# Optimization experiments

Hardware: AMD Instinct MI355X
Metric: run time of the kernel (lower is better)

The kernel has to match this reference:

```python
import jax, jax.numpy as jnp
import numpy as np
import math

B, S, D, H = 2, 2048, 1024, 16
DH = D // H  # head_dim = 64
NEG = -10000.0


def setup_inputs() -> dict:
    key = jax.random.key(0)
    ks = jax.random.split(key, 6)
    scale = 1.0 / math.sqrt(D)
    inp = {
        "query": jax.random.normal(ks[0], (B, S, D), dtype=jnp.float32),
        "key": jax.random.normal(ks[1], (B, S, D), dtype=jnp.float32),
        "value": jax.random.normal(ks[2], (B, S, D), dtype=jnp.float32),
        "Wq": jax.random.normal(ks[3], (D, D), dtype=jnp.float32) * scale,
        "Wk": jax.random.normal(ks[4], (D, D), dtype=jnp.float32) * scale,
        "Wv": jax.random.normal(ks[5], (D, D), dtype=jnp.float32) * scale,
        "pad_mask": jnp.ones((B, 1, 1, S), dtype=jnp.int32),
        "attn_mask": jnp.tril(jnp.ones((S, S), dtype=jnp.int32))[None, None],  # causal [1,1,S,S]
    }
    return inp


def reference(query, key, value, Wq, Wk, Wv, pad_mask, attn_mask):
    b, s, d = query.shape
    # torch Linear(bias=False): y = x @ W.T ; then split into heads [B,H,S,DH]
    def proj(x, W):
        return (x @ W.T).reshape(b, -1, H, DH).transpose(0, 2, 1, 3)

    Q = proj(query, Wq)
    K = proj(key, Wk)
    V = proj(value, Wv)

    scores = jnp.einsum("bhqd,bhkd->bhqk", Q, K) / math.sqrt(DH)
    scores = jnp.where(attn_mask == 0, NEG, scores)
    scores = jnp.where(pad_mask == 0, NEG, scores)
    attn = jax.nn.softmax(scores, axis=-1)  # dropout p=0.0 -> identity
    ctx = jnp.einsum("bhqk,bhkd->bhqd", attn, V)
    return ctx.transpose(0, 2, 1, 3).reshape(b, -1, d)
```

## Files before the change

### kernel.cpp

```cpp
#include <hip/hip_runtime.h>


typedef unsigned short u16;
typedef unsigned int u32;
typedef u16 u16x4 __attribute__((ext_vector_type(4)));
typedef u16 u16x8 __attribute__((ext_vector_type(8)));
typedef u32 u32x2 __attribute__((ext_vector_type(2)));
typedef u32 u32x4 __attribute__((ext_vector_type(4)));
typedef __bf16 bf16x8 __attribute__((ext_vector_type(8)));
typedef float f32x4 __attribute__((ext_vector_type(4)));

static __device__ __forceinline__ u16 f2bf(float f) {
  unsigned u = __builtin_bit_cast(unsigned, f);
  return (u16)((u + 0x7FFFu + ((u >> 16) & 1u)) >> 16);
}

static __device__ __forceinline__ u32 cvt_pk_bf16(float lo, float hi) {
  u32 r;
  asm("v_cvt_pk_bf16_f32 %0, %1, %2" : "=v"(r) : "v"(lo), "v"(hi));
  return r;
}

static __device__ __forceinline__ u16x8 cvt8(float4 f0, float4 f1) {
  u32x4 v;
  v[0] = cvt_pk_bf16(f0.x, f0.y);
  v[1] = cvt_pk_bf16(f0.z, f0.w);
  v[2] = cvt_pk_bf16(f1.x, f1.y);
  v[3] = cvt_pk_bf16(f1.z, f1.w);
  return __builtin_bit_cast(u16x8, v);
}

static __device__ __forceinline__ f32x4 mfma16(u16x8 a, u16x8 b, f32x4 c) {
  return __builtin_amdgcn_mfma_f32_16x16x32_bf16(
      __builtin_bit_cast(bf16x8, a), __builtin_bit_cast(bf16x8, b), c, 0, 0, 0);
}

#define GLOAD16(GSRC, LDST)                                                  \
  __builtin_amdgcn_global_load_lds(                                         \
      (const __attribute__((address_space(1))) unsigned int*)(GSRC),        \
      (__attribute__((address_space(3))) unsigned int*)(LDST), 16, 0, 0)

#define FENCE() asm volatile("" ::: "memory")
#define BARX()                        \
  do {                                \
    __builtin_amdgcn_s_barrier();     \
    FENCE();                          \
  } while (0)

__global__ __launch_bounds__(256) void wconv_kernel(
    const float* __restrict__ Wq, const float* __restrict__ Wk,
    const float* __restrict__ Wv, u16* __restrict__ dst) {
  const float* src = (blockIdx.y == 0) ? Wq : (blockIdx.y == 1) ? Wk : Wv;
  u16* d = dst + (size_t)blockIdx.y * (1024 * 1024);
  const int i = (blockIdx.x * 256 + threadIdx.x) * 8;
  const float4 f0 = *(const float4*)(src + i);
  const float4 f1 = *(const float4*)(src + i + 4);
  *(u16x8*)(d + i) = cvt8(f0, f1);
}

__global__ __launch_bounds__(256) void proj_kernel(
    const float* __restrict__ Xq, const float* __restrict__ Xk, const float* __restrict__ Xv,
    const u16* __restrict__ Wbf,
    u16* __restrict__ Qb, u16* __restrict__ Kb, u16* __restrict__ Vt) {
  const int d0 = blockIdx.x;
  const int tid = (d0 & 7) * 96 + (d0 >> 3);
  const int nI = tid % 24, mI = tid / 24;
  const int mode = nI >> 3;
  const int m0 = mI * 128;
  const int n0 = (nI & 7) * 128;

  const float* __restrict__ X = (mode == 0) ? Xq : (mode == 1) ? Xk : Xv;
  const u16* __restrict__ W = Wbf + (size_t)mode * (1024 * 1024);

  __shared__ __align__(16) u16 As[3][128 * 32];
  __shared__ __align__(16) u16 Bs[3][128 * 32];

  const int t = threadIdx.x;
  const int lane = t & 63;
  const int w = t >> 6;
  const int wm = w >> 1, wn = w & 1;
  const int lr = lane & 15, lg = lane >> 4;

  const int srow0 = w * 32 + (lane >> 2);
  const int srow1 = srow0 + 16;
  const int skoff = ((lane & 3) ^ ((lane >> 3) & 3)) * 8;
  const int ldsb0 = w * 2048 + lane * 16;
  const int ldsb1 = ldsb0 + 1024;

  const float* Xr0 = X + (size_t)(m0 + srow0) * 1024 + skoff;
  const float* Xr1 = X + (size_t)(m0 + srow1) * 1024 + skoff;
  const u16* Wr0 = W + (size_t)(n0 + srow0) * 1024 + skoff;
  const u16* Wr1 = W + (size_t)(n0 + srow1) * 1024 + skoff;

  float4 a0_, a1_, a2_, a3_;

#define ISSUE_A(T)                                   \
  do {                                               \
    const float* _p0 = Xr0 + (T) * 32;               \
    const float* _p1 = Xr1 + (T) * 32;               \
    a0_ = ((const float4*)_p0)[0];                   \
    a1_ = ((const float4*)_p0)[1];                   \
    a2_ = ((const float4*)_p1)[0];                   \
    a3_ = ((const float4*)_p1)[1];                   \
  } while (0)
#define WRITE_A(BUF)                                                 \
  do {                                                               \
    *(u16x8*)((char*)As[BUF] + ldsb0) = cvt8(a0_, a1_);              \
    *(u16x8*)((char*)As[BUF] + ldsb1) = cvt8(a2_, a3_);              \
  } while (0)
#define ISSUE_B(T, BUF)                                              \
  do {                                                               \
    GLOAD16(Wr0 + (T) * 32, (char*)Bs[BUF] + w * 2048);              \
    GLOAD16(Wr1 + (T) * 32, (char*)Bs[BUF] + w * 2048 + 1024);       \
  } while (0)

  f32x4 acc[4][4] = {};
  const int rx = (lr >> 1) & 3;

#define CMP(BUF)                                                              \
  do {                                                                       \
    u16x8 af[4], bfr[4];                                                     \
    _Pragma("unroll") for (int mi = 0; mi < 4; ++mi) {                        \
      const int row = wm * 64 + mi * 16 + lr;                                \
      af[mi] = *(const u16x8*)((char*)As[BUF] + row * 64 + ((lg ^ rx) << 4)); \
    }                                                                         \
    _Pragma("unroll") for (int ni = 0; ni < 4; ++ni) {                        \
      const int row = wn * 64 + ni * 16 + lr;                                \
      bfr[ni] = *(const u16x8*)((char*)Bs[BUF] + row * 64 + ((lg ^ rx) << 4));\
    }                                                                         \
    _Pragma("unroll") for (int mi = 0; mi < 4; ++mi)                          \
        _Pragma("unroll") for (int ni = 0; ni < 4; ++ni)                      \
            acc[mi][ni] = mfma16(af[mi], bfr[ni], acc[mi][ni]);               \
  } while (0)

  ISSUE_A(0); WRITE_A(0);
  ISSUE_A(1); WRITE_A(1);
  ISSUE_A(2);
  ISSUE_B(0, 0);
  ISSUE_B(1, 1);
  asm volatile("s_waitcnt vmcnt(2) lgkmcnt(0)" ::: "memory");
  BARX();

  CMP(0);
  BARX();
  WRITE_A(2);
  ISSUE_A(3);
  ISSUE_B(2, 2);

  for (int tt = 1; tt <= 29; ++tt) {
    asm volatile("s_waitcnt vmcnt(6) lgkmcnt(0)" ::: "memory");
    BARX();
    CMP(tt % 3);
    BARX();
    WRITE_A((tt + 2) % 3);
    if (tt < 29) ISSUE_A(tt + 3);
    ISSUE_B(tt + 2, (tt + 2) % 3);
  }

  asm volatile("s_waitcnt vmcnt(2) lgkmcnt(0)" ::: "memory");
  BARX();
  CMP(30 % 3);
  asm volatile("s_waitcnt vmcnt(0) lgkmcnt(0)" ::: "memory");
  BARX();
  CMP(31 % 3);
#undef ISSUE_A
#undef WRITE_A
#undef ISSUE_B
#undef CMP

#pragma unroll
  for (int mi = 0; mi < 4; ++mi) {
    const int sbase = m0 + wm * 64 + mi * 16 + lg * 4;
    const int b_ = sbase >> 11;
    const int s_ = sbase & 2047;
#pragma unroll
    for (int ni = 0; ni < 4; ++ni) {
      const int n = n0 + wn * 64 + ni * 16 + lr;
      const int h_ = n >> 6, dh = n & 63;
      if (mode == 2) {
        u16x4 pk;
        pk[0] = f2bf(acc[mi][ni][0]);
        pk[1] = f2bf(acc[mi][ni][1]);
        pk[2] = f2bf(acc[mi][ni][2]);
        pk[3] = f2bf(acc[mi][ni][3]);
        *(u16x4*)(Vt + ((size_t)((b_ * 16 + h_) * 64 + dh)) * 2048 + s_) = pk;
      } else {
        const float sc = (mode == 0) ? 0.18033688f : 1.0f;
        u16* dst = (mode == 0 ? Qb : Kb) + (size_t)(b_ * 16 + h_) * (2048 * 64) + dh;
#pragma unroll
        for (int r = 0; r < 4; ++r)
          dst[(size_t)(s_ + r) * 64] = f2bf(acc[mi][ni][r] * sc);
      }
    }
  }
}

__global__ __launch_bounds__(256, 4) void attn_kernel(
    const u16* __restrict__ Qb, const u16* __restrict__ Kb, const u16* __restrict__ Vt,
    const int* __restrict__ pad, float* __restrict__ out) {
  const int bh = blockIdx.x;
  const int qb = blockIdx.y;
  const int b = bh >> 4, h = bh & 15;
  const int q0 = qb * 64;
  const u16* Qh = Qb + (size_t)bh * (2048 * 64);
  const u16* Kh = Kb + (size_t)bh * (2048 * 64);
  const u16* Vh = Vt + (size_t)bh * (64 * 2048);
  const int* padb = pad + b * 2048;

  __shared__ u16 Ks[2][64 * 64];
  __shared__ u16 Vs[2][64 * 64];
  __shared__ u16 Ps[4][16 * 64];

  const int t = threadIdx.x, lane = t & 63, w = t >> 6;
  const int lr = lane & 15, lg = lane >> 4;
  const int swz = (lr & 7) << 4;
  const int sr = t >> 3, scb = t & 7;
  const int qwave = q0 + w * 16;
  const int qlane = qwave + lr;
  const int nsteps = qb + 1;

  u16x8 qf[2];
#pragma unroll
  for (int kc = 0; kc < 2; ++kc)
    qf[kc] = *(const u16x8*)(Qh + (size_t)qlane * 64 + kc * 32 + lg * 8);

  f32x4 acc[4] = {};
  float mrow = -1e4f, lsum = 0.f;

  u16x8 kr0, kr1, vr0, vr1;
  const int sb0 = (sr * 128 + scb * 16) ^ ((sr & 7) << 4);
  const int sb1 = ((32 + sr) * 128 + scb * 16) ^ ((sr & 7) << 4);

  kr0 = *(const u16x8*)(Kh + (size_t)sr * 64 + scb * 8);
  kr1 = *(const u16x8*)(Kh + (size_t)(32 + sr) * 64 + scb * 8);
  vr0 = *(const u16x8*)(Vh + (size_t)sr * 2048 + scb * 8);
  vr1 = *(const u16x8*)(Vh + (size_t)(32 + sr) * 2048 + scb * 8);
  *(u16x8*)((char*)Ks[0] + sb0) = kr0;
  *(u16x8*)((char*)Ks[0] + sb1) = kr1;
  *(u16x8*)((char*)Vs[0] + sb0) = vr0;
  *(u16x8*)((char*)Vs[0] + sb1) = vr1;
  __syncthreads();

  int cur = 0;
  for (int st = 0; st < nsteps; ++st) {
    const int kv0 = st << 6;
    const bool more = st + 1 < nsteps;
    if (more) {
      const int nv0 = kv0 + 64;
      kr0 = *(const u16x8*)(Kh + (size_t)(nv0 + sr) * 64 + scb * 8);
      kr1 = *(const u16x8*)(Kh + (size_t)(nv0 + 32 + sr) * 64 + scb * 8);
      vr0 = *(const u16x8*)(Vh + (size_t)sr * 2048 + nv0 + scb * 8);
      vr1 = *(const u16x8*)(Vh + (size_t)(32 + sr) * 2048 + nv0 + scb * 8);
    }
    int4 pv4[4];
#pragma unroll
    for (int ct = 0; ct < 4; ++ct)
      pv4[ct] = *(const int4*)(padb + kv0 + ct * 16 + lg * 4);

    const u16* KsC = Ks[cur];
    const u16* VsC = Vs[cur];

    f32x4 s4[4] = {};
#pragma unroll
    for (int ct = 0; ct < 4; ++ct) {
      if (kv0 + ct * 16 <= qwave + 15) {
#pragma unroll
        for (int kc = 0; kc < 2; ++kc) {
          const int byt = ((ct * 16 + lr) * 128 + kc * 64 + lg * 16) ^ swz;
          const u16x8 kf = *(const u16x8*)((char*)KsC + byt);
          s4[ct] = mfma16(kf, qf[kc], s4[ct]);
        }
      }
    }

    float vv[4][4];
    const int pall = pv4[0].x & pv4[0].y & pv4[0].z & pv4[0].w &
                     pv4[1].x & pv4[1].y & pv4[1].z & pv4[1].w &
                     pv4[2].x & pv4[2].y & pv4[2].z & pv4[2].w &
                     pv4[3].x & pv4[3].y & pv4[3].z & pv4[3].w;
    if ((kv0 + 63 <= qwave) && __all(pall != 0)) {
#pragma unroll
      for (int ct = 0; ct < 4; ++ct)
#pragma unroll
        for (int r = 0; r < 4; ++r) vv[ct][r] = s4[ct][r];
    } else {
      const int lim = qlane - kv0 - lg * 4;
#pragma unroll
      for (int ct = 0; ct < 4; ++ct) {
        const int* pvp = (const int*)&pv4[ct];
#pragma unroll
        for (int r = 0; r < 4; ++r)
          vv[ct][r] = (pvp[r] && (ct * 16 + r) <= lim) ? s4[ct][r] : -1e4f;
      }
    }

    float m0 = fmaxf(fmaxf(fmaxf(vv[0][0], vv[0][1]), fmaxf(vv[0][2], vv[0][3])),
                     fmaxf(fmaxf(vv[1][0], vv[1][1]), fmaxf(vv[1][2], vv[1][3])));
    float m1 = fmaxf(fmaxf(fmaxf(vv[2][0], vv[2][1]), fmaxf(vv[2][2], vv[2][3])),
                     fmaxf(fmaxf(vv[3][0], vv[3][1]), fmaxf(vv[3][2], vv[3][3])));
    float mx = fmaxf(m0, m1);
    mx = fmaxf(mx, __shfl_xor(mx, 16));
    mx = fmaxf(mx, __shfl_xor(mx, 32));
    const float mn = fmaxf(mrow, mx);
    const float al = exp2f(mrow - mn);
    mrow = mn;

    float p[4][4];
#pragma unroll
    for (int ct = 0; ct < 4; ++ct)
#pragma unroll
      for (int r = 0; r < 4; ++r) p[ct][r] = exp2f(vv[ct][r] - mn);
    float ps = (((p[0][0] + p[0][1]) + (p[0][2] + p[0][3])) +
                ((p[1][0] + p[1][1]) + (p[1][2] + p[1][3]))) +
               (((p[2][0] + p[2][1]) + (p[2][2] + p[2][3])) +
                ((p[3][0] + p[3][1]) + (p[3][2] + p[3][3])));
    ps += __shfl_xor(ps, 16);
    ps += __shfl_xor(ps, 32);
    lsum = lsum * al + ps;

    u16* PsB = &Ps[w][0];
#pragma unroll
    for (int ct = 0; ct < 4; ++ct) {
      u32x2 pw;
      pw[0] = cvt_pk_bf16(p[ct][0], p[ct][1]);
      pw[1] = cvt_pk_bf16(p[ct][2], p[ct][3]);
      const int pb = (lr * 128 + ct * 32 + lg * 8) ^ swz;
      *(u32x2*)((char*)PsB + pb) = pw;
    }
    const u16x8 pa0 = *(const u16x8*)((char*)PsB + ((lr * 128 + lg * 16) ^ swz));
    const u16x8 pa1 = *(const u16x8*)((char*)PsB + ((lr * 128 + 64 + lg * 16) ^ swz));

    float alv[4];
#pragma unroll
    for (int r = 0; r < 4; ++r)
      alv[r] = __builtin_bit_cast(
          float, __builtin_amdgcn_ds_bpermute((lg * 4 + r) * 4, __builtin_bit_cast(int, al)));

#pragma unroll
    for (int dt = 0; dt < 4; ++dt) {
#pragma unroll
      for (int r = 0; r < 4; ++r) acc[dt][r] *= alv[r];
      const int r0 = (dt * 16 + lr) * 128;
      acc[dt] = mfma16(pa0, *(const u16x8*)((char*)VsC + ((r0 + lg * 16) ^ swz)), acc[dt]);
      acc[dt] = mfma16(pa1, *(const u16x8*)((char*)VsC + ((r0 + 64 + lg * 16) ^ swz)), acc[dt]);
    }

    if (more) {
      u16* Kn = Ks[cur ^ 1];
      u16* Vn = Vs[cur ^ 1];
      *(u16x8*)((char*)Kn + sb0) = kr0;
      *(u16x8*)((char*)Kn + sb1) = kr1;
      *(u16x8*)((char*)Vn + sb0) = vr0;
      *(u16x8*)((char*)Vn + sb1) = vr1;
    }
    __syncthreads();
    cur ^= 1;
  }

  const float il = 1.0f / lsum;
  float linv[4];
#pragma unroll
  for (int r = 0; r < 4; ++r)
    linv[r] = __builtin_bit_cast(
        float, __builtin_amdgcn_ds_bpermute((lg * 4 + r) * 4, __builtin_bit_cast(int, il)));
  float* obase = out + ((size_t)(b * 2048 + qwave + lg * 4)) * 1024 + h * 64 + lr;
#pragma unroll
  for (int r = 0; r < 4; ++r)
#pragma unroll
    for (int dt = 0; dt < 4; ++dt)
      obase[(size_t)r * 1024 + dt * 16] = acc[dt][r] * linv[r];
}

extern "C" void kernel_launch(void* const* d_in, const int* in_sizes, int n_in,
                              void* d_out, int out_size, void* d_ws, size_t ws_size,
                              hipStream_t stream) {
  const float* q  = (const float*)d_in[0];
  const float* k  = (const float*)d_in[1];
  const float* v  = (const float*)d_in[2];
  const float* wq = (const float*)d_in[3];
  const float* wk = (const float*)d_in[4];
  const float* wv = (const float*)d_in[5];
  const int* pad  = (const int*)d_in[6];
  float* out = (float*)d_out;

  u16* Qb  = (u16*)d_ws;
  u16* Kb  = Qb + (size_t)4 * 1024 * 1024;
  u16* Vt  = Kb + (size_t)4 * 1024 * 1024;
  u16* Wbf = Vt + (size_t)4 * 1024 * 1024;

  dim3 gc(512, 3);
  wconv_kernel<<<gc, 256, 0, stream>>>(wq, wk, wv, Wbf);

  proj_kernel<<<768, 256, 0, stream>>>(q, k, v, Wbf, Qb, Kb, Vt);

  dim3 ga(32, 32);
  attn_kernel<<<ga, 256, 0, stream>>>(Qb, Kb, Vt, pad, out);
}
```

Before: 113.8 us.

## Pair causal query blocks per CTA and add lazy softmax rescaling

Each attention block now handles two query tiles, a long one (31-pi) and a short one (pi). This balances causal work across blocks and lets both tiles share each staged K/V tile in LDS. The online softmax skips the accumulator rescale unless the row max grows by more than 8 in log2 units, and the MFMA phases are wrapped in s_setprio. The change doubles per-thread accumulator and Q-fragment registers, so launch bounds are lowered to 2 blocks per SM, which reduces occupancy.

```diff
diff --git a/kernel.cpp b/kernel.cpp
--- a/kernel.cpp
+++ b/kernel.cpp
@@ -33,6 +33,11 @@
 static __device__ __forceinline__ f32x4 mfma16(u16x8 a, u16x8 b, f32x4 c) {
   return __builtin_amdgcn_mfma_f32_16x16x32_bf16(
       __builtin_bit_cast(bf16x8, a), __builtin_bit_cast(bf16x8, b), c, 0, 0, 0);
+}
+
+static __device__ __forceinline__ float bperm_f(int lane, float v) {
+  return __builtin_bit_cast(
+      float, __builtin_amdgcn_ds_bpermute(lane * 4, __builtin_bit_cast(int, v)));
 }
 
 #define GLOAD16(GSRC, LDST)                                                  \
@@ -195,13 +200,17 @@
   }
 }
 
-__global__ __launch_bounds__(256, 4) void attn_kernel(
+__global__ __launch_bounds__(256, 2) void attn_kernel(
     const u16* __restrict__ Qb, const u16* __restrict__ Kb, const u16* __restrict__ Vt,
     const int* __restrict__ pad, float* __restrict__ out) {
-  const int bh = blockIdx.x;
-  const int qb = blockIdx.y;
+  const int id = blockIdx.x;
+  const int g = id >> 8, r_ = id & 255;
+  const int bh = r_ & 31;
+  const int p8 = r_ >> 5;
+  const int pi = g ? (15 - p8) : p8;
+  const int qbA = 31 - pi, qbB = pi;
+
   const int b = bh >> 4, h = bh & 15;
-  const int q0 = qb * 64;
   const u16* Qh = Qb + (size_t)bh * (2048 * 64);
   const u16* Kh = Kb + (size_t)bh * (2048 * 64);
   const u16* Vh = Vt + (size_t)bh * (64 * 2048);
@@ -215,17 +224,17 @@
   const int lr = lane & 15, lg = lane >> 4;
   const int swz = (lr & 7) << 4;
   const int sr = t >> 3, scb = t & 7;
-  const int qwave = q0 + w * 16;
-  const int qlane = qwave + lr;
-  const int nsteps = qb + 1;
-
-  u16x8 qf[2];
-#pragma unroll
-  for (int kc = 0; kc < 2; ++kc)
-    qf[kc] = *(const u16x8*)(Qh + (size_t)qlane * 64 + kc * 32 + lg * 8);
-
-  f32x4 acc[4] = {};
-  float mrow = -1e4f, lsum = 0.f;
+  const int qwaveA = qbA * 64 + w * 16, qwaveB = qbB * 64 + w * 16;
+
+  u16x8 qfA[2], qfB[2];
+#pragma unroll
+  for (int kc = 0; kc < 2; ++kc) {
+    qfA[kc] = *(const u16x8*)(Qh + (size_t)(qwaveA + lr) * 64 + kc * 32 + lg * 8);
+    qfB[kc] = *(const u16x8*)(Qh + (size_t)(qwaveB + lr) * 64 + kc * 32 + lg * 8);
+  }
+
+  f32x4 accA[4] = {}, accB[4] = {};
+  float mrowA = -1e4f, lsumA = 0.f, mrowB = -1e4f, lsumB = 0.f;
 
   u16x8 kr0, kr1, vr0, vr1;
   const int sb0 = (sr * 128 + scb * 16) ^ ((sr & 7) << 4);
@@ -241,10 +250,86 @@
   *(u16x8*)((char*)Vs[0] + sb1) = vr1;
   __syncthreads();
 
+#define PROCESS(QF, ACC, MROW, LSUM, QWAVE)                                    \
+  do {                                                                         \
+    f32x4 s4[4] = {};                                                          \
+    __builtin_amdgcn_s_setprio(1);                                             \
+    _Pragma("unroll") for (int ct = 0; ct < 4; ++ct) {                         \
+      if (kv0 + ct * 16 <= (QWAVE) + 15) {                                     \
+        _Pragma("unroll") for (int kc = 0; kc < 2; ++kc) {                     \
+          const int byt = ((ct * 16 + lr) * 128 + kc * 64 + lg * 16) ^ swz;    \
+          const u16x8 kf = *(const u16x8*)((char*)KsC + byt);                  \
+          s4[ct] = mfma16(kf, QF[kc], s4[ct]);                                 \
+        }                                                                      \
+      }                                                                        \
+    }                                                                          \
+    __builtin_amdgcn_s_setprio(0);                                             \
+    float vv[4][4];                                                            \
+    if ((kv0 + 63 <= (QWAVE)) && allpad) {                                     \
+      _Pragma("unroll") for (int ct = 0; ct < 4; ++ct)                         \
+          _Pragma("unroll") for (int rr = 0; rr < 4; ++rr)                     \
+              vv[ct][rr] = s4[ct][rr];                                         \
+    } else {                                                                   \
+      const int lim = (QWAVE) + lr - kv0 - lg * 4;                             \
+      _Pragma("unroll") for (int ct = 0; ct < 4; ++ct) {                       \
+        const int* pvp = (const int*)&pv4[ct];                                 \
+        _Pragma("unroll") for (int rr = 0; rr < 4; ++rr)                       \
+            vv[ct][rr] = (pvp[rr] && (ct * 16 + rr) <= lim) ? s4[ct][rr]       \
+                                                            : -1e4f;           \
+      }                                                                        \
+    }                                                                          \
+    float m0_ = fmaxf(fmaxf(fmaxf(vv[0][0], vv[0][1]), fmaxf(vv[0][2], vv[0][3])), \
+                      fmaxf(fmaxf(vv[1][0], vv[1][1]), fmaxf(vv[1][2], vv[1][3]))); \
+    float m1_ = fmaxf(fmaxf(fmaxf(vv[2][0], vv[2][1]), fmaxf(vv[2][2], vv[2][3])), \
+                      fmaxf(fmaxf(vv[3][0], vv[3][1]), fmaxf(vv[3][2], vv[3][3]))); \
+    float mx = fmaxf(m0_, m1_);                                                \
+    mx = fmaxf(mx, __shfl_xor(mx, 16));                                        \
+    mx = fmaxf(mx, __shfl_xor(mx, 32));                                        \
+    if (!__all(mx <= (MROW) + 8.0f)) { \
+      const float mn = fmaxf((MROW), mx);                                      \
+      const float al = exp2f((MROW) - mn);                                     \
+      (MROW) = mn;                                                             \
+      (LSUM) *= al;                                                            \
+      _Pragma("unroll") for (int rr = 0; rr < 4; ++rr) {                       \
+        const float alv = bperm_f(lg * 4 + rr, al);                            \
+        _Pragma("unroll") for (int dt = 0; dt < 4; ++dt) ACC[dt][rr] *= alv;   \
+      }                                                                        \
+    }                                                                          \
+    float p[4][4];                                                             \
+    _Pragma("unroll") for (int ct = 0; ct < 4; ++ct)                           \
+        _Pragma("unroll") for (int rr = 0; rr < 4; ++rr)                       \
+            p[ct][rr] = exp2f(vv[ct][rr] - (MROW));                            \
+    float ps = (((p[0][0] + p[0][1]) + (p[0][2] + p[0][3])) +                  \
+                ((p[1][0] + p[1][1]) + (p[1][2] + p[1][3]))) +                 \
+               (((p[2][0] + p[2][1]) + (p[2][2] + p[2][3])) +                  \
+                ((p[3][0] + p[3][1]) + (p[3][2] + p[3][3])));                  \
+    ps += __shfl_xor(ps, 16);                                                  \
+    ps += __shfl_xor(ps, 32);                                                  \
+    (LSUM) += ps;                                                              \
+    u16* PsB = &Ps[w][0];                                                      \
+    _Pragma("unroll") for (int ct = 0; ct < 4; ++ct) {                         \
+      u32x2 pw;                                                                \
+      pw[0] = cvt_pk_bf16(p[ct][0], p[ct][1]);                                 \
+      pw[1] = cvt_pk_bf16(p[ct][2], p[ct][3]);                                 \
+      const int pb = (lr * 128 + ct * 32 + lg * 8) ^ swz;                      \
+      *(u32x2*)((char*)PsB + pb) = pw;                                         \
+    }                                                                          \
+    const u16x8 pa0 = *(const u16x8*)((char*)PsB + ((lr * 128 + lg * 16) ^ swz));      \
+    const u16x8 pa1 = *(const u16x8*)((char*)PsB + ((lr * 128 + 64 + lg * 16) ^ swz)); \
+    __builtin_amdgcn_s_setprio(1);                                             \
+    _Pragma("unroll") for (int dt = 0; dt < 4; ++dt) {                         \
+      const int r0 = (dt * 16 + lr) * 128;                                     \
+      ACC[dt] = mfma16(pa0, *(const u16x8*)((char*)VsC + ((r0 + lg * 16) ^ swz)), ACC[dt]);      \
+      ACC[dt] = mfma16(pa1, *(const u16x8*)((char*)VsC + ((r0 + 64 + lg * 16) ^ swz)), ACC[dt]); \
+    }                                                                          \
+    __builtin_amdgcn_s_setprio(0);                                             \
+  } while (0)
+
   int cur = 0;
-  for (int st = 0; st < nsteps; ++st) {
+  const int nst = qbA + 1;
+  for (int st = 0; st < nst; ++st) {
     const int kv0 = st << 6;
-    const bool more = st + 1 < nsteps;
+    const bool more = st + 1 < nst;
     if (more) {
       const int nv0 = kv0 + 64;
       kr0 = *(const u16x8*)(Kh + (size_t)(nv0 + sr) * 64 + scb * 8);
@@ -256,94 +341,18 @@
 #pragma unroll
     for (int ct = 0; ct < 4; ++ct)
       pv4[ct] = *(const int4*)(padb + kv0 + ct * 16 + lg * 4);
-
-    const u16* KsC = Ks[cur];
-    const u16* VsC = Vs[cur];
-
-    f32x4 s4[4] = {};
-#pragma unroll
-    for (int ct = 0; ct < 4; ++ct) {
-      if (kv0 + ct * 16 <= qwave + 15) {
-#pragma unroll
-        for (int kc = 0; kc < 2; ++kc) {
-          const int byt = ((ct * 16 + lr) * 128 + kc * 64 + lg * 16) ^ swz;
-          const u16x8 kf = *(const u16x8*)((char*)KsC + byt);
-          s4[ct] = mfma16(kf, qf[kc], s4[ct]);
-        }
-      }
-    }
-
-    float vv[4][4];
     const int pall = pv4[0].x & pv4[0].y & pv4[0].z & pv4[0].w &
                      pv4[1].x & pv4[1].y & pv4[1].z & pv4[1].w &
                      pv4[2].x & pv4[2].y & pv4[2].z & pv4[2].w &
                      pv4[3].x & pv4[3].y & pv4[3].z & pv4[3].w;
-    if ((kv0 + 63 <= qwave) && __all(pall != 0)) {
-#pragma unroll
-      for (int ct = 0; ct < 4; ++ct)
-#pragma unroll
-        for (int r = 0; r < 4; ++r) vv[ct][r] = s4[ct][r];
-    } else {
-      const int lim = qlane - kv0 - lg * 4;
-#pragma unroll
-      for (int ct = 0; ct < 4; ++ct) {
-        const int* pvp = (const int*)&pv4[ct];
-#pragma unroll
-        for (int r = 0; r < 4; ++r)
-          vv[ct][r] = (pvp[r] && (ct * 16 + r) <= lim) ? s4[ct][r] : -1e4f;
-      }
-    }
-
-    float m0 = fmaxf(fmaxf(fmaxf(vv[0][0], vv[0][1]), fmaxf(vv[0][2], vv[0][3])),
-                     fmaxf(fmaxf(vv[1][0], vv[1][1]), fmaxf(vv[1][2], vv[1][3])));
-    float m1 = fmaxf(fmaxf(fmaxf(vv[2][0], vv[2][1]), fmaxf(vv[2][2], vv[2][3])),
-                     fmaxf(fmaxf(vv[3][0], vv[3][1]), fmaxf(vv[3][2], vv[3][3])));
-    float mx = fmaxf(m0, m1);
-    mx = fmaxf(mx, __shfl_xor(mx, 16));
-    mx = fmaxf(mx, __shfl_xor(mx, 32));
-    const float mn = fmaxf(mrow, mx);
-    const float al = exp2f(mrow - mn);
-    mrow = mn;
-
-    float p[4][4];
-#pragma unroll
-    for (int ct = 0; ct < 4; ++ct)
-#pragma unroll
-      for (int r = 0; r < 4; ++r) p[ct][r] = exp2f(vv[ct][r] - mn);
-    float ps = (((p[0][0] + p[0][1]) + (p[0][2] + p[0][3])) +
-                ((p[1][0] + p[1][1]) + (p[1][2] + p[1][3]))) +
-               (((p[2][0] + p[2][1]) + (p[2][2] + p[2][3])) +
-                ((p[3][0] + p[3][1]) + (p[3][2] + p[3][3])));
-    ps += __shfl_xor(ps, 16);
-    ps += __shfl_xor(ps, 32);
-    lsum = lsum * al + ps;
-
-    u16* PsB = &Ps[w][0];
-#pragma unroll
-    for (int ct = 0; ct < 4; ++ct) {
-      u32x2 pw;
-      pw[0] = cvt_pk_bf16(p[ct][0], p[ct][1]);
-      pw[1] = cvt_pk_bf16(p[ct][2], p[ct][3]);
-      const int pb = (lr * 128 + ct * 32 + lg * 8) ^ swz;
-      *(u32x2*)((char*)PsB + pb) = pw;
-    }
-    const u16x8 pa0 = *(const u16x8*)((char*)PsB + ((lr * 128 + lg * 16) ^ swz));
-    const u16x8 pa1 = *(const u16x8*)((char*)PsB + ((lr * 128 + 64 + lg * 16) ^ swz));
-
-    float alv[4];
-#pragma unroll
-    for (int r = 0; r < 4; ++r)
-      alv[r] = __builtin_bit_cast(
-          float, __builtin_amdgcn_ds_bpermute((lg * 4 + r) * 4, __builtin_bit_cast(int, al)));
-
-#pragma unroll
-    for (int dt = 0; dt < 4; ++dt) {
-#pragma unroll
-      for (int r = 0; r < 4; ++r) acc[dt][r] *= alv[r];
-      const int r0 = (dt * 16 + lr) * 128;
-      acc[dt] = mfma16(pa0, *(const u16x8*)((char*)VsC + ((r0 + lg * 16) ^ swz)), acc[dt]);
-      acc[dt] = mfma16(pa1, *(const u16x8*)((char*)VsC + ((r0 + 64 + lg * 16) ^ swz)), acc[dt]);
-    }
+    const bool allpad = __all(pall != 0);
+
+    const u16* KsC = Ks[cur];
+    const u16* VsC = Vs[cur];
+
+    PROCESS(qfA, accA, mrowA, lsumA, qwaveA);
+    if (st <= qbB)
+      PROCESS(qfB, accB, mrowB, lsumB, qwaveB);
 
     if (more) {
       u16* Kn = Ks[cur ^ 1];
@@ -356,19 +365,23 @@
     __syncthreads();
     cur ^= 1;
   }
-
-  const float il = 1.0f / lsum;
-  float linv[4];
-#pragma unroll
-  for (int r = 0; r < 4; ++r)
-    linv[r] = __builtin_bit_cast(
-        float, __builtin_amdgcn_ds_bpermute((lg * 4 + r) * 4, __builtin_bit_cast(int, il)));
-  float* obase = out + ((size_t)(b * 2048 + qwave + lg * 4)) * 1024 + h * 64 + lr;
-#pragma unroll
-  for (int r = 0; r < 4; ++r)
-#pragma unroll
-    for (int dt = 0; dt < 4; ++dt)
-      obase[(size_t)r * 1024 + dt * 16] = acc[dt][r] * linv[r];
+#undef PROCESS
+
+#pragma unroll
+  for (int tile = 0; tile < 2; ++tile) {
+    const f32x4* acc = tile ? accB : accA;
+    const float lsum = tile ? lsumB : lsumA;
+    const int qwave = tile ? qwaveB : qwaveA;
+    const float il = 1.0f / lsum;
+    float* obase = out + ((size_t)(b * 2048 + qwave + lg * 4)) * 1024 + h * 64 + lr;
+#pragma unroll
+    for (int r = 0; r < 4; ++r) {
+      const float linv = bperm_f(lg * 4 + r, il);
+#pragma unroll
+      for (int dt = 0; dt < 4; ++dt)
+        obase[(size_t)r * 1024 + dt * 16] = acc[dt][r] * linv;
+    }
+  }
 }
 
 extern "C" void kernel_launch(void* const* d_in, const int* in_sizes, int n_in,
@@ -393,6 +406,5 @@
 
   proj_kernel<<<768, 256, 0, stream>>>(q, k, v, Wbf, Qb, Kb, Vt);
 
-  dim3 ga(32, 32);
-  attn_kernel<<<ga, 256, 0, stream>>>(Qb, Kb, Vt, pad, out);
-}
+  attn_kernel<<<512, 256, 0, stream>>>(Qb, Kb, Vt, pad, out);
+}
```

Measured after the change: 98.98 us. -13.0%, faster.
